# Performance work log

Hardware: AMD Instinct MI355X
Metric: run time of the kernel (lower is better)

Reference implementation:

```python
import jax, jax.numpy as jnp
import numpy as np

DEPTH = 8  # dilation_depth; dilation for layer i is 2**(i % DEPTH)


def causal_conv(x, w, b, dilation):
    # x: [B,C,T], w: [O,I,K] -> causal dilated conv, output [B,O,T]
    pad = (w.shape[-1] - 1) * dilation
    xp = jnp.pad(x, ((0, 0), (0, 0), (pad, 0)))
    y = jax.lax.conv_general_dilated(
        xp, w, window_strides=(1,), padding='VALID',
        rhs_dilation=(dilation,), dimension_numbers=('NCW', 'OIW', 'NCW'))
    return y + b[None, :, None]


def conv1x1(x, w, b):
    # x: [B,C,T], w: [O,C] -> [B,O,T]
    return jnp.einsum('oc,bct->bot', w, x) + b[None, :, None]


def setup_inputs() -> dict:
    key = jax.random.key(0)
    ks = jax.random.split(key, 20)
    B, T, F, E = 16, 2048, 32, 16
    R, S, O, NOUT, L = 256, 128, 64, 24, 32  # residual, skip, out_size, n_output, layers
    s = 0.05
    return {
        'X_batch': jax.random.normal(ks[0], (B, T, F), jnp.float32),
        'X_batch_ex': jax.random.normal(ks[1], (B, E), jnp.float32),
        'w_in': jax.random.normal(ks[2], (R, F, 2), jnp.float32) * s,
        'b_in': jax.random.normal(ks[3], (R,), jnp.float32) * s,
        'w_filter': jax.random.normal(ks[4], (L, R, R, 2), jnp.float32) * s,
        'b_filter': jax.random.normal(ks[5], (L, R), jnp.float32) * s,
        'w_gate': jax.random.normal(ks[6], (L, R, R, 2), jnp.float32) * s,
        'b_gate': jax.random.normal(ks[7], (L, R), jnp.float32) * s,
        'w_res': jax.random.normal(ks[8], (L, R, R), jnp.float32) * s,
        'b_res': jax.random.normal(ks[9], (L, R), jnp.float32) * s,
        'w_skip': jax.random.normal(ks[10], (L, S, R), jnp.float32) * s,
        'b_skip': jax.random.normal(ks[11], (L, S), jnp.float32) * s,
        'w_out1': jax.random.normal(ks[12], (O, S), jnp.float32) * s,
        'b_out1': jax.random.normal(ks[13], (O,), jnp.float32) * s,
        'w_out2': jax.random.normal(ks[14], (O, O), jnp.float32) * s,
        'b_out2': jax.random.normal(ks[15], (O,), jnp.float32) * s,
        'w_lin': jax.random.normal(ks[16], (NOUT, O + E), jnp.float32) * s,
        'b_lin': jax.random.normal(ks[17], (NOUT,), jnp.float32) * s,
    }


def reference(X_batch, X_batch_ex, w_in, b_in, w_filter, b_filter, w_gate, b_gate,
              w_res, b_res, w_skip, b_skip, w_out1, b_out1, w_out2, b_out2,
              w_lin, b_lin):
    # [B,T,F] -> [B,F,T]
    x = jnp.transpose(X_batch, (0, 2, 1))
    x = causal_conv(x, w_in, b_in, 1)
    L = w_filter.shape[0]
    skip_sum = jnp.zeros((x.shape[0], w_skip.shape[1], x.shape[2]), x.dtype)
    for i in range(L):
        d = 2 ** (i % DEPTH)
        f = jnp.tanh(causal_conv(x, w_filter[i], b_filter[i], d))
        g = jax.nn.sigmoid(causal_conv(x, w_gate[i], b_gate[i], d))
        fx = conv1x1(f * g, w_res[i], b_res[i])
        skip_sum = skip_sum + conv1x1(fx, w_skip[i], b_skip[i])
        x = fx + x
    out = jax.nn.relu(skip_sum)
    out = jax.nn.relu(conv1x1(out, w_out1, b_out1))
    out = conv1x1(out, w_out2, b_out2)          # [B,O,T]
    h = out[:, :, -1]                            # last timestep, [B,O]
    h = jnp.concatenate([h, X_batch_ex], axis=1)
    h = jax.nn.relu(h)
    return h @ w_lin.T + b_lin                   # [B, n_output]
```

## Files before the change

kernel.cpp:

```cpp
#include <hip/hip_runtime.h>
#include <cmath>

#define TBUF 1024
#define RCH  256

typedef __bf16 bf16x8 __attribute__((ext_vector_type(8)));
typedef float  f32x4  __attribute__((ext_vector_type(4)));

__device__ inline unsigned short f2bf(float f) {
  unsigned u = __builtin_bit_cast(unsigned, f);
  u += 0x7FFFu + ((u >> 16) & 1u);
  return (unsigned short)(u >> 16);
}
__device__ inline float bf2f(unsigned short h) {
  unsigned u = ((unsigned)h) << 16;
  return __builtin_bit_cast(float, u);
}

__global__ __launch_bounds__(256) void prep(
    const float* __restrict__ wf, const float* __restrict__ wg,
    const float* __restrict__ wr, const float* __restrict__ wsk,
    const float* __restrict__ w_in,
    unsigned short* __restrict__ Wb, unsigned short* __restrict__ Wrb,
    float* __restrict__ wskT, float* __restrict__ w2)
{
  const int bid = blockIdx.x;
  const int tid = threadIdx.x;
  if (bid < 16384) {
    int idx = bid * 256 + tid;
    int c  = idx & 255;
    int op = (idx >> 8) & 511;
    int i  = idx >> 17;
    int o  = op & 255;
    const float* src = (op < 256) ? wf : wg;
    const float2 v = *(const float2*)&src[(((size_t)i * 256 + o) * 256 + c) << 1];
    unsigned short* dst = Wb + ((size_t)i * 512 + op) * 512;
    dst[c]       = f2bf(v.y);
    dst[256 + c] = f2bf(v.x);
  } else if (bid < 18432) {
    int idx = (bid - 16384) * 256 + tid;
    float4 v = ((const float4*)wr)[idx];
    uint2 o;
    o.x = (unsigned)f2bf(v.x) | ((unsigned)f2bf(v.y) << 16);
    o.y = (unsigned)f2bf(v.z) | ((unsigned)f2bf(v.w) << 16);
    ((uint2*)Wrb)[idx] = o;
  } else if (bid < 22528) {
    int idx = (bid - 18432) * 256 + tid;
    int s = idx & 127;
    int c = (idx >> 7) & 255;
    int i = idx >> 15;
    wskT[idx] = wsk[(i * 128 + s) * 256 + c];
  } else {
    int idx = (bid - 22528) * 256 + tid;
    int r = idx & 255;
    int fk = idx >> 8;
    int f = fk & 31, k = fk >> 5;
    w2[idx] = w_in[r * 64 + f * 2 + k];
  }
}

__global__ __launch_bounds__(256) void in_conv(
    const float* __restrict__ X, const float* __restrict__ w2,
    const float* __restrict__ b_in, unsigned short* __restrict__ xbb,
    unsigned short* __restrict__ xlo)
{
  const int bid   = blockIdx.x;
  const int b     = bid & 15;
  const int chunk = bid >> 4;
  const int r     = threadIdx.x;
  __shared__ float Xs[17][32];
  const int tt0 = chunk << 4;
  const int t0  = tt0 + 1024;
  for (int idx = r; idx < 17 * 32; idx += 256) {
    int row = idx >> 5, f = idx & 31;
    Xs[row][f] = X[((size_t)b * 2048 + (t0 - 1 + row)) * 32 + f];
  }
  __syncthreads();
  float w0[32], w1[32];
  #pragma unroll
  for (int f = 0; f < 32; ++f) {
    w0[f] = w2[f * 256 + r];
    w1[f] = w2[(32 + f) * 256 + r];
  }
  const float bias = b_in[r];
  float4 prev[8], cur[8];
  #pragma unroll
  for (int q = 0; q < 8; ++q) prev[q] = *(const float4*)&Xs[0][q * 4];
  #pragma unroll
  for (int j = 0; j < 16; ++j) {
    #pragma unroll
    for (int q = 0; q < 8; ++q) cur[q] = *(const float4*)&Xs[j + 1][q * 4];
    float a = bias;
    #pragma unroll
    for (int q = 0; q < 8; ++q) {
      a = fmaf(w0[q*4+0], prev[q].x, a); a = fmaf(w1[q*4+0], cur[q].x, a);
      a = fmaf(w0[q*4+1], prev[q].y, a); a = fmaf(w1[q*4+1], cur[q].y, a);
      a = fmaf(w0[q*4+2], prev[q].z, a); a = fmaf(w1[q*4+2], cur[q].z, a);
      a = fmaf(w0[q*4+3], prev[q].w, a); a = fmaf(w1[q*4+3], cur[q].w, a);
    }
    int tt = tt0 + j;
    size_t off = ((size_t)b * TBUF + tt) * RCH + r;
    if (tt < 3) { xbb[off] = 0; xlo[off] = 0; }
    else {
      unsigned short hn = f2bf(a);
      xbb[off] = hn;
      xlo[off] = f2bf(a - bf2f(hn));
    }
    #pragma unroll
    for (int q = 0; q < 8; ++q) prev[q] = cur[q];
  }
}

template<int NM>
__global__ __launch_bounds__(1024, 4) void layer_fused(
    const unsigned short* __restrict__ xbb_r, unsigned short* __restrict__ xbb_w,
    unsigned short* __restrict__ xlo,
    const unsigned short* __restrict__ Wb,
    const unsigned short* __restrict__ Wrb,
    const float* __restrict__ bF, const float* __restrict__ bG,
    const float* __restrict__ bR,
    int dd, int t_lo, float* __restrict__ fxs_i)
{
  __shared__ __align__(16) unsigned short As[NM * 16 * 520];
  const int bid  = blockIdx.x;
  const int b    = bid & 15;
  const int tile = bid >> 4;
  const int tid  = threadIdx.x;
  const int w    = tid >> 6;
  const int lane = tid & 63;
  const int l15  = lane & 15;
  const int lk8  = (lane >> 4) << 3;
  const int rr0  = (lane >> 4) << 2;
  const int tt0  = t_lo + tile * (NM * 16);
  const unsigned short* xB = xbb_r + ((size_t)b << 18);

  {
    const int c   = lane;
    const int tap = c >> 5;
    const int cg  = (c & 31) << 3;
    #pragma unroll
    for (int it = 0; it < NM; ++it) {
      int r = it * 16 + w;
      int tt = tt0 + r - tap * dd;
      tt = min(max(tt, 0), 1023);
      __builtin_amdgcn_global_load_lds(
          (const __attribute__((address_space(1))) unsigned int*)
              (xB + ((size_t)tt << 8) + cg),
          (__attribute__((address_space(3))) unsigned int*)
              ((char*)As + r * 1040),
          16, 0, 0);
    }
  }

  const unsigned short* wf0 = Wb + (size_t)(16 * w + l15) * 512 + lk8;
  const unsigned short* wg0 = wf0 + (size_t)256 * 512;
  const unsigned short* wr0 = Wrb + (size_t)(16 * w + l15) * 256 + lk8;
  uint4 nbf = *(const uint4*)(wf0);
  uint4 nbg = *(const uint4*)(wg0);
  uint4 nr0 = *(const uint4*)(wr0);
  __syncthreads();

  f32x4 accf[NM] = {};
  f32x4 accg[NM] = {};
  #pragma unroll 4
  for (int kc = 0; kc < 16; ++kc) {
    uint4 cbf = nbf, cbg = nbg;
    if (kc < 15) {
      nbf = *(const uint4*)(wf0 + (kc + 1) * 32);
      nbg = *(const uint4*)(wg0 + (kc + 1) * 32);
    }
    const int colb = (kc * 32 + lk8) * 2;
    bf16x8 a[NM];
    #pragma unroll
    for (int mf = 0; mf < NM; ++mf)
      a[mf] = *(const bf16x8*)((const char*)As + (mf * 16 + l15) * 1040 + colb);
    bf16x8 vf0 = __builtin_bit_cast(bf16x8, cbf);
    bf16x8 vg0 = __builtin_bit_cast(bf16x8, cbg);
    #pragma unroll
    for (int mf = 0; mf < NM; ++mf) {
      accf[mf] = __builtin_amdgcn_mfma_f32_16x16x32_bf16(a[mf], vf0, accf[mf], 0, 0, 0);
      accg[mf] = __builtin_amdgcn_mfma_f32_16x16x32_bf16(a[mf], vg0, accg[mf], 0, 0, 0);
    }
  }

  const int col = 16 * w + l15;
  float hi_pre[NM][4];
  #pragma unroll
  for (int mf = 0; mf < NM; ++mf)
    #pragma unroll
    for (int j = 0; j < 4; ++j) {
      int row = mf * 16 + rr0 + j;
      hi_pre[mf][j] = bf2f(*(const unsigned short*)((const char*)As + row * 1040 + col * 2));
    }

  unsigned short* xL = xlo + ((size_t)b << 18);
  float lo_pre[NM][4];
  #pragma unroll
  for (int mf = 0; mf < NM; ++mf)
    #pragma unroll
    for (int j = 0; j < 4; ++j) {
      int tt = min(tt0 + mf * 16 + rr0 + j, 1023);
      lo_pre[mf][j] = bf2f(xL[((size_t)tt << 8) + col]);
    }
  __syncthreads();

  unsigned short* Zs = As;
  const float bfv = bF[col];
  const float bgv = bG[col];
  #pragma unroll
  for (int mf = 0; mf < NM; ++mf)
    #pragma unroll
    for (int j = 0; j < 4; ++j) {
      int row = mf * 16 + rr0 + j;
      float pf = accf[mf][j] + bfv;
      float pg = accg[mf][j] + bgv;
      float e2 = __expf(2.f * pf);
      float th = 1.f - 2.f / (e2 + 1.f);
      float sg = 1.f / (1.f + __expf(-pg));
      *(unsigned short*)((char*)Zs + row * 528 + col * 2) = f2bf(th * sg);
    }
  __syncthreads();

  f32x4 acc[NM] = {};
  #pragma unroll 4
  for (int kc = 0; kc < 8; ++kc) {
    uint4 cr0 = nr0;
    if (kc < 7) nr0 = *(const uint4*)(wr0 + (kc + 1) * 32);
    const int colb = (kc * 32 + lk8) * 2;
    bf16x8 a[NM];
    #pragma unroll
    for (int mf = 0; mf < NM; ++mf)
      a[mf] = *(const bf16x8*)((const char*)Zs + (mf * 16 + l15) * 528 + colb);
    bf16x8 v0 = __builtin_bit_cast(bf16x8, cr0);
    #pragma unroll
    for (int mf = 0; mf < NM; ++mf)
      acc[mf] = __builtin_amdgcn_mfma_f32_16x16x32_bf16(a[mf], v0, acc[mf], 0, 0, 0);
  }

  const float brv = bR[col];
  unsigned short* xBb = xbb_w + ((size_t)b << 18);
  #pragma unroll
  for (int mf = 0; mf < NM; ++mf)
    #pragma unroll
    for (int j = 0; j < 4; ++j) {
      int tt = tt0 + mf * 16 + rr0 + j;
      if (tt > 1023) continue;
      size_t off = ((size_t)tt << 8) + col;
      float fx = acc[mf][j] + brv;
      float xn = (hi_pre[mf][j] + lo_pre[mf][j]) + fx;
      unsigned short hn = f2bf(xn);
      xBb[off] = hn;
      xL[off]  = f2bf(xn - bf2f(hn));
      if (tt == 1023) fxs_i[(size_t)b * 256 + col] = fx;
    }
}

__global__ __launch_bounds__(128) void skip_partial(
    const float* __restrict__ fxs, const float* __restrict__ wskT,
    const float* __restrict__ b_skip, float* __restrict__ part)
{
  int i = blockIdx.x, b = blockIdx.y, s = threadIdx.x;
  __shared__ float fxsh[256];
  fxsh[s]       = fxs[((size_t)i * 16 + b) * 256 + s];
  fxsh[s + 128] = fxs[((size_t)i * 16 + b) * 256 + s + 128];
  __syncthreads();
  float a = b_skip[i * 128 + s];
  const float* wp = wskT + (size_t)i * 256 * 128 + s;
  #pragma unroll 4
  for (int c = 0; c < 256; c++)
    a = fmaf(wp[c * 128], fxsh[c], a);
  part[((size_t)i * 16 + b) * 128 + s] = a;
}

__global__ __launch_bounds__(128) void head2(
    const float* __restrict__ part, const float* __restrict__ w_o1,
    const float* __restrict__ b_o1, const float* __restrict__ w_o2,
    const float* __restrict__ b_o2, const float* __restrict__ w_lin,
    const float* __restrict__ b_lin, const float* __restrict__ Xex,
    float* __restrict__ out)
{
  int b = blockIdx.x, tid = threadIdx.x;
  __shared__ float sk[128];
  __shared__ float h1[64];
  __shared__ float hc[80];
  float a = 0.f;
  for (int i = 0; i < 32; i++) a += part[((size_t)i * 16 + b) * 128 + tid];
  sk[tid] = fmaxf(a, 0.f);
  __syncthreads();
  if (tid < 64) {
    float a1 = b_o1[tid];
    for (int s = 0; s < 128; s++) a1 = fmaf(w_o1[tid * 128 + s], sk[s], a1);
    h1[tid] = fmaxf(a1, 0.f);
  }
  __syncthreads();
  if (tid < 64) {
    float a2 = b_o2[tid];
    for (int j = 0; j < 64; j++) a2 = fmaf(w_o2[tid * 64 + j], h1[j], a2);
    hc[tid] = fmaxf(a2, 0.f);
  }
  if (tid >= 64 && tid < 80) hc[tid] = fmaxf(Xex[b * 16 + (tid - 64)], 0.f);
  __syncthreads();
  if (tid < 24) {
    float a3 = b_lin[tid];
    for (int j = 0; j < 80; j++) a3 = fmaf(w_lin[tid * 80 + j], hc[j], a3);
    out[b * 24 + tid] = a3;
  }
}

extern "C" void kernel_launch(void* const* d_in, const int* in_sizes, int n_in,
                              void* d_out, int out_size, void* d_ws, size_t ws_size,
                              hipStream_t stream)
{
  (void)in_sizes; (void)n_in; (void)out_size; (void)ws_size;
  const float* X     = (const float*)d_in[0];
  const float* Xex   = (const float*)d_in[1];
  const float* w_in  = (const float*)d_in[2];
  const float* b_in  = (const float*)d_in[3];
  const float* w_f   = (const float*)d_in[4];
  const float* b_f   = (const float*)d_in[5];
  const float* w_g   = (const float*)d_in[6];
  const float* b_g   = (const float*)d_in[7];
  const float* w_r   = (const float*)d_in[8];
  const float* b_r   = (const float*)d_in[9];
  const float* w_s   = (const float*)d_in[10];
  const float* b_s   = (const float*)d_in[11];
  const float* w_o1  = (const float*)d_in[12];
  const float* b_o1  = (const float*)d_in[13];
  const float* w_o2  = (const float*)d_in[14];
  const float* b_o2  = (const float*)d_in[15];
  const float* w_lin = (const float*)d_in[16];
  const float* b_lin = (const float*)d_in[17];

  float* ws   = (float*)d_ws;
  float* wskT = ws;
  float* fxs  = wskT + 1048576;
  float* part = fxs  + 131072;
  float* w2   = part + 65536;
  unsigned short* Wb   = (unsigned short*)(w2 + 16384);
  unsigned short* Wrb  = Wb   + 8388608;
  unsigned short* xbbA = Wrb  + 2097152;
  unsigned short* xbbB = xbbA + 4194304;
  unsigned short* xlo  = xbbB + 4194304;

  prep<<<22592, 256, 0, stream>>>(w_f, w_g, w_r, w_s, w_in, Wb, Wrb, wskT, w2);
  in_conv<<<1024, 256, 0, stream>>>(X, w2, b_in, xbbA, xlo);

  static const int wI[33] = {1021,1020,1018,1014,1006,990,958,894,
                             766,765,763,759,751,735,703,639,
                             511,510,508,504,496,480,448,384,
                             256,255,253,249,241,225,193,129,1};
  for (int i = 0; i < 32; i++) {
    int dd    = 1 << (i & 7);
    int Wout  = wI[i + 1];
    int t_lo  = TBUF - Wout;
    unsigned short* xin  = (i & 1) ? xbbB : xbbA;
    unsigned short* xout = (i & 1) ? xbbA : xbbB;
    const unsigned short* WbL  = Wb  + (size_t)i * 512 * 512;
    const unsigned short* WrbL = Wrb + (size_t)i * 256 * 256;
    const float* bFi = b_f + i * 256;
    const float* bGi = b_g + i * 256;
    const float* bRi = b_r + i * 256;
    float* fxi = fxs + (size_t)i * 16 * 256;
    int NM = (Wout + 255) >> 8;
    int tiles = (Wout + NM * 16 - 1) / (NM * 16);
    switch (NM) {
      case 4:
        layer_fused<4><<<tiles * 16, 1024, 0, stream>>>(
            xin, xout, xlo, WbL, WrbL, bFi, bGi, bRi, dd, t_lo, fxi);
        break;
      case 3:
        layer_fused<3><<<tiles * 16, 1024, 0, stream>>>(
            xin, xout, xlo, WbL, WrbL, bFi, bGi, bRi, dd, t_lo, fxi);
        break;
      case 2:
        layer_fused<2><<<tiles * 16, 1024, 0, stream>>>(
            xin, xout, xlo, WbL, WrbL, bFi, bGi, bRi, dd, t_lo, fxi);
        break;
      default:
        layer_fused<1><<<tiles * 16, 1024, 0, stream>>>(
            xin, xout, xlo, WbL, WrbL, bFi, bGi, bRi, dd, t_lo, fxi);
        break;
    }
  }
  skip_partial<<<dim3(32, 16), 128, 0, stream>>>(fxs, wskT, b_s, part);
  head2<<<16, 128, 0, stream>>>(part, w_o1, b_o1, w_o2, b_o2, w_lin, b_lin, Xex, (float*)d_out);
}
```

Measured before the change: 883.0 us.

## Fuse pairs of small-dilation WaveNet layers into one kernel with halo recompute

Adds a layer_pair kernel that computes two consecutive residual layers (dilation 1→2 and 4→8) in one launch. It recomputes a 16-row halo of the first layer's output in shared memory, so the intermediate activation never goes through global memory. This cuts launches and global traffic for those layer pairs. In exchange it does redundant halo computation, uses more LDS per block, and double-buffers the lo buffer. The intermediate is kept only in bf16 (the lo part is dropped), which may change precision slightly.

```diff
diff --git a/kernel.cpp b/kernel.cpp
--- a/kernel.cpp
+++ b/kernel.cpp
@@ -15,6 +15,11 @@
 __device__ inline float bf2f(unsigned short h) {
   unsigned u = ((unsigned)h) << 16;
   return __builtin_bit_cast(float, u);
+}
+__device__ __forceinline__ void gl2lds(const unsigned short* g, void* l) {
+  __builtin_amdgcn_global_load_lds(
+      (const __attribute__((address_space(1))) unsigned int*)g,
+      (__attribute__((address_space(3))) unsigned int*)l, 16, 0, 0);
 }
 
 __global__ __launch_bounds__(256) void prep(
@@ -143,15 +148,9 @@
       int r = it * 16 + w;
       int tt = tt0 + r - tap * dd;
       tt = min(max(tt, 0), 1023);
-      __builtin_amdgcn_global_load_lds(
-          (const __attribute__((address_space(1))) unsigned int*)
-              (xB + ((size_t)tt << 8) + cg),
-          (__attribute__((address_space(3))) unsigned int*)
-              ((char*)As + r * 1040),
-          16, 0, 0);
-    }
-  }
-
+      gl2lds(xB + ((size_t)tt << 8) + cg, (char*)As + r * 1040);
+    }
+  }
   const unsigned short* wf0 = Wb + (size_t)(16 * w + l15) * 512 + lk8;
   const unsigned short* wg0 = wf0 + (size_t)256 * 512;
   const unsigned short* wr0 = Wrb + (size_t)(16 * w + l15) * 256 + lk8;
@@ -192,7 +191,6 @@
       int row = mf * 16 + rr0 + j;
       hi_pre[mf][j] = bf2f(*(const unsigned short*)((const char*)As + row * 1040 + col * 2));
     }
-
   unsigned short* xL = xlo + ((size_t)b << 18);
   float lo_pre[NM][4];
   #pragma unroll
@@ -253,6 +251,221 @@
       xL[off]  = f2bf(xn - bf2f(hn));
       if (tt == 1023) fxs_i[(size_t)b * 256 + col] = fx;
     }
+}
+
+template<int D2>
+__global__ __launch_bounds__(1024, 4) void layer_pair(
+    const unsigned short* __restrict__ xhi_r, unsigned short* __restrict__ xhi_w,
+    const unsigned short* __restrict__ xlo_r, unsigned short* __restrict__ xlo_w,
+    const unsigned short* __restrict__ Wb1, const unsigned short* __restrict__ Wrb1,
+    const unsigned short* __restrict__ Wb2, const unsigned short* __restrict__ Wrb2,
+    const float* __restrict__ bF1, const float* __restrict__ bG1,
+    const float* __restrict__ bR1, const float* __restrict__ bF2,
+    const float* __restrict__ bG2, const float* __restrict__ bR2,
+    int dd1, int t_lo2, float* __restrict__ fxs1, float* __restrict__ fxs2)
+{
+  __shared__ __align__(16) unsigned short R1[80 * 520];
+  __shared__ __align__(16) unsigned short R2[80 * 260];
+  const int bid  = blockIdx.x;
+  const int b    = bid & 15;
+  const int tile = bid >> 4;
+  const int tid  = threadIdx.x;
+  const int w    = tid >> 6;
+  const int lane = tid & 63;
+  const int l15  = lane & 15;
+  const int lk8  = (lane >> 4) << 3;
+  const int rr0  = (lane >> 4) << 2;
+  const int tt0e = t_lo2 + tile * 64 - 16;
+  const unsigned short* xH = xhi_r + ((size_t)b << 18);
+  const unsigned short* xL = xlo_r + ((size_t)b << 18);
+
+  {
+    const int c   = lane;
+    const int tap = c >> 5;
+    const int cg  = (c & 31) << 3;
+    #pragma unroll
+    for (int it = 0; it < 5; ++it) {
+      int r = it * 16 + w;
+      int tt = tt0e + r - tap * dd1;
+      tt = min(max(tt, 0), 1023);
+      gl2lds(xH + ((size_t)tt << 8) + cg, (char*)R1 + r * 1040);
+    }
+  }
+  const unsigned short* wf1 = Wb1 + (size_t)(16 * w + l15) * 512 + lk8;
+  const unsigned short* wg1 = wf1 + (size_t)256 * 512;
+  const unsigned short* wr1 = Wrb1 + (size_t)(16 * w + l15) * 256 + lk8;
+  uint4 nbf = *(const uint4*)(wf1);
+  uint4 nbg = *(const uint4*)(wg1);
+  uint4 nr  = *(const uint4*)(wr1);
+  __syncthreads();
+
+  f32x4 accf[5] = {};
+  f32x4 accg[5] = {};
+  #pragma unroll 4
+  for (int kc = 0; kc < 16; ++kc) {
+    uint4 cbf = nbf, cbg = nbg;
+    if (kc < 15) {
+      nbf = *(const uint4*)(wf1 + (kc + 1) * 32);
+      nbg = *(const uint4*)(wg1 + (kc + 1) * 32);
+    }
+    const int colb = (kc * 32 + lk8) * 2;
+    bf16x8 a[5];
+    #pragma unroll
+    for (int mf = 0; mf < 5; ++mf)
+      a[mf] = *(const bf16x8*)((const char*)R1 + (mf * 16 + l15) * 1040 + colb);
+    bf16x8 vf0 = __builtin_bit_cast(bf16x8, cbf);
+    bf16x8 vg0 = __builtin_bit_cast(bf16x8, cbg);
+    #pragma unroll
+    for (int mf = 0; mf < 5; ++mf) {
+      accf[mf] = __builtin_amdgcn_mfma_f32_16x16x32_bf16(a[mf], vf0, accf[mf], 0, 0, 0);
+      accg[mf] = __builtin_amdgcn_mfma_f32_16x16x32_bf16(a[mf], vg0, accg[mf], 0, 0, 0);
+    }
+  }
+
+  const int col = 16 * w + l15;
+  float hi_pre[5][4], lo_pre[5][4];
+  #pragma unroll
+  for (int mf = 0; mf < 5; ++mf)
+    #pragma unroll
+    for (int j = 0; j < 4; ++j) {
+      int row = mf * 16 + rr0 + j;
+      hi_pre[mf][j] = bf2f(*(const unsigned short*)((const char*)R1 + row * 1040 + col * 2));
+      int tt = min(max(tt0e + row, 0), 1023);
+      lo_pre[mf][j] = bf2f(xL[((size_t)tt << 8) + col]);
+    }
+  __syncthreads();
+
+  {
+    const float bfv = bF1[col], bgv = bG1[col];
+    #pragma unroll
+    for (int mf = 0; mf < 5; ++mf)
+      #pragma unroll
+      for (int j = 0; j < 4; ++j) {
+        int row = mf * 16 + rr0 + j;
+        float pf = accf[mf][j] + bfv;
+        float pg = accg[mf][j] + bgv;
+        float e2 = __expf(2.f * pf);
+        float th = 1.f - 2.f / (e2 + 1.f);
+        float sg = 1.f / (1.f + __expf(-pg));
+        *(unsigned short*)((char*)R1 + row * 528 + col * 2) = f2bf(th * sg);
+      }
+  }
+  __syncthreads();
+
+  float xn1[5][4];
+  {
+    f32x4 acc1[5] = {};
+    #pragma unroll 4
+    for (int kc = 0; kc < 8; ++kc) {
+      uint4 cr = nr;
+      if (kc < 7) nr = *(const uint4*)(wr1 + (kc + 1) * 32);
+      const int colb = (kc * 32 + lk8) * 2;
+      bf16x8 a[5];
+      #pragma unroll
+      for (int mf = 0; mf < 5; ++mf)
+        a[mf] = *(const bf16x8*)((const char*)R1 + (mf * 16 + l15) * 528 + colb);
+      bf16x8 v0 = __builtin_bit_cast(bf16x8, cr);
+      #pragma unroll
+      for (int mf = 0; mf < 5; ++mf)
+        acc1[mf] = __builtin_amdgcn_mfma_f32_16x16x32_bf16(a[mf], v0, acc1[mf], 0, 0, 0);
+    }
+    const float br1 = bR1[col];
+    #pragma unroll
+    for (int mf = 0; mf < 5; ++mf)
+      #pragma unroll
+      for (int j = 0; j < 4; ++j) {
+        int row = mf * 16 + rr0 + j;
+        float fx = acc1[mf][j] + br1;
+        float xn = (hi_pre[mf][j] + lo_pre[mf][j]) + fx;
+        xn1[mf][j] = xn;
+        *(unsigned short*)((char*)R2 + row * 520 + col * 2) = f2bf(xn);
+        if (tt0e + row == 1023) fxs1[(size_t)b * 256 + col] = fx;
+      }
+  }
+  const unsigned short* wf2 = Wb2 + (size_t)(16 * w + l15) * 512 + lk8;
+  const unsigned short* wg2 = wf2 + (size_t)256 * 512;
+  const unsigned short* wr2 = Wrb2 + (size_t)(16 * w + l15) * 256 + lk8;
+  nbf = *(const uint4*)(wf2);
+  nbg = *(const uint4*)(wg2);
+  __syncthreads();
+
+  f32x4 acc2f[4] = {};
+  f32x4 acc2g[4] = {};
+  #pragma unroll 4
+  for (int kc = 0; kc < 16; ++kc) {
+    uint4 cbf = nbf, cbg = nbg;
+    if (kc < 15) {
+      nbf = *(const uint4*)(wf2 + (kc + 1) * 32);
+      nbg = *(const uint4*)(wg2 + (kc + 1) * 32);
+    }
+    const int tapofs = (kc >= 8) ? D2 : 0;
+    const int colb = ((kc & 7) * 32 + lk8) * 2;
+    bf16x8 a[4];
+    #pragma unroll
+    for (int mf = 0; mf < 4; ++mf)
+      a[mf] = *(const bf16x8*)((const char*)R2 + (16 + mf * 16 + l15 - tapofs) * 520 + colb);
+    bf16x8 vf0 = __builtin_bit_cast(bf16x8, cbf);
+    bf16x8 vg0 = __builtin_bit_cast(bf16x8, cbg);
+    #pragma unroll
+    for (int mf = 0; mf < 4; ++mf) {
+      acc2f[mf] = __builtin_amdgcn_mfma_f32_16x16x32_bf16(a[mf], vf0, acc2f[mf], 0, 0, 0);
+      acc2g[mf] = __builtin_amdgcn_mfma_f32_16x16x32_bf16(a[mf], vg0, acc2g[mf], 0, 0, 0);
+    }
+  }
+  nr = *(const uint4*)(wr2);
+
+  {
+    const float bfv = bF2[col], bgv = bG2[col];
+    #pragma unroll
+    for (int mf = 0; mf < 4; ++mf)
+      #pragma unroll
+      for (int j = 0; j < 4; ++j) {
+        int row = mf * 16 + rr0 + j;
+        float pf = acc2f[mf][j] + bfv;
+        float pg = acc2g[mf][j] + bgv;
+        float e2 = __expf(2.f * pf);
+        float th = 1.f - 2.f / (e2 + 1.f);
+        float sg = 1.f / (1.f + __expf(-pg));
+        *(unsigned short*)((char*)R1 + row * 528 + col * 2) = f2bf(th * sg);
+      }
+  }
+  __syncthreads();
+
+  {
+    f32x4 acc2[4] = {};
+    #pragma unroll 4
+    for (int kc = 0; kc < 8; ++kc) {
+      uint4 cr = nr;
+      if (kc < 7) nr = *(const uint4*)(wr2 + (kc + 1) * 32);
+      const int colb = (kc * 32 + lk8) * 2;
+      bf16x8 a[4];
+      #pragma unroll
+      for (int mf = 0; mf < 4; ++mf)
+        a[mf] = *(const bf16x8*)((const char*)R1 + (mf * 16 + l15) * 528 + colb);
+      bf16x8 v0 = __builtin_bit_cast(bf16x8, cr);
+      #pragma unroll
+      for (int mf = 0; mf < 4; ++mf)
+        acc2[mf] = __builtin_amdgcn_mfma_f32_16x16x32_bf16(a[mf], v0, acc2[mf], 0, 0, 0);
+    }
+    const float br2 = bR2[col];
+    unsigned short* oH = xhi_w + ((size_t)b << 18);
+    unsigned short* oL = xlo_w + ((size_t)b << 18);
+    #pragma unroll
+    for (int mf = 0; mf < 4; ++mf)
+      #pragma unroll
+      for (int j = 0; j < 4; ++j) {
+        int row = 16 + mf * 16 + rr0 + j;
+        int tt = tt0e + row;
+        if (tt > 1023) continue;
+        size_t off = ((size_t)tt << 8) + col;
+        float fx2 = acc2[mf][j] + br2;
+        float xn2 = xn1[mf + 1][j] + fx2;
+        unsigned short hn = f2bf(xn2);
+        oH[off] = hn;
+        oL[off] = f2bf(xn2 - bf2f(hn));
+        if (tt == 1023) fxs2[(size_t)b * 256 + col] = fx2;
+      }
+  }
 }
 
 __global__ __launch_bounds__(128) void skip_partial(
@@ -338,48 +551,72 @@
   float* w2   = part + 65536;
   unsigned short* Wb   = (unsigned short*)(w2 + 16384);
   unsigned short* Wrb  = Wb   + 8388608;
-  unsigned short* xbbA = Wrb  + 2097152;
-  unsigned short* xbbB = xbbA + 4194304;
-  unsigned short* xlo  = xbbB + 4194304;
+  unsigned short* hiA  = Wrb  + 2097152;
+  unsigned short* hiB  = hiA  + 4194304;
+  unsigned short* loA  = hiB  + 4194304;
+  unsigned short* loB  = loA  + 4194304;
 
   prep<<<22592, 256, 0, stream>>>(w_f, w_g, w_r, w_s, w_in, Wb, Wrb, wskT, w2);
-  in_conv<<<1024, 256, 0, stream>>>(X, w2, b_in, xbbA, xlo);
+  in_conv<<<1024, 256, 0, stream>>>(X, w2, b_in, hiA, loA);
 
   static const int wI[33] = {1021,1020,1018,1014,1006,990,958,894,
                              766,765,763,759,751,735,703,639,
                              511,510,508,504,496,480,448,384,
                              256,255,253,249,241,225,193,129,1};
-  for (int i = 0; i < 32; i++) {
-    int dd    = 1 << (i & 7);
-    int Wout  = wI[i + 1];
-    int t_lo  = TBUF - Wout;
-    unsigned short* xin  = (i & 1) ? xbbB : xbbA;
-    unsigned short* xout = (i & 1) ? xbbA : xbbB;
-    const unsigned short* WbL  = Wb  + (size_t)i * 512 * 512;
-    const unsigned short* WrbL = Wrb + (size_t)i * 256 * 256;
-    const float* bFi = b_f + i * 256;
-    const float* bGi = b_g + i * 256;
-    const float* bRi = b_r + i * 256;
-    float* fxi = fxs + (size_t)i * 16 * 256;
-    int NM = (Wout + 255) >> 8;
-    int tiles = (Wout + NM * 16 - 1) / (NM * 16);
-    switch (NM) {
-      case 4:
-        layer_fused<4><<<tiles * 16, 1024, 0, stream>>>(
-            xin, xout, xlo, WbL, WrbL, bFi, bGi, bRi, dd, t_lo, fxi);
-        break;
-      case 3:
-        layer_fused<3><<<tiles * 16, 1024, 0, stream>>>(
-            xin, xout, xlo, WbL, WrbL, bFi, bGi, bRi, dd, t_lo, fxi);
-        break;
-      case 2:
-        layer_fused<2><<<tiles * 16, 1024, 0, stream>>>(
-            xin, xout, xlo, WbL, WrbL, bFi, bGi, bRi, dd, t_lo, fxi);
-        break;
-      default:
-        layer_fused<1><<<tiles * 16, 1024, 0, stream>>>(
-            xin, xout, xlo, WbL, WrbL, bFi, bGi, bRi, dd, t_lo, fxi);
-        break;
+  unsigned short* hi_c = hiA; unsigned short* hi_n = hiB;
+  unsigned short* lo_c = loA; unsigned short* lo_n = loB;
+  int i = 0;
+  while (i < 32) {
+    const int m = i & 7;
+    if (m == 0 || m == 2) {
+      const int d2   = 1 << ((i + 1) & 7);
+      const int dd1  = 1 << m;
+      const int W2   = wI[i + 2];
+      const int t_lo2 = TBUF - W2;
+      const int tiles = (W2 + 63) / 64;
+      if (d2 == 2)
+        layer_pair<2><<<tiles * 16, 1024, 0, stream>>>(
+            hi_c, hi_n, lo_c, lo_n,
+            Wb + (size_t)i * 262144, Wrb + (size_t)i * 65536,
+            Wb + (size_t)(i + 1) * 262144, Wrb + (size_t)(i + 1) * 65536,
+            b_f + i * 256, b_g + i * 256, b_r + i * 256,
+            b_f + (i + 1) * 256, b_g + (i + 1) * 256, b_r + (i + 1) * 256,
+            dd1, t_lo2, fxs + (size_t)i * 4096, fxs + (size_t)(i + 1) * 4096);
+      else
+        layer_pair<8><<<tiles * 16, 1024, 0, stream>>>(
+            hi_c, hi_n, lo_c, lo_n,
+            Wb + (size_t)i * 262144, Wrb + (size_t)i * 65536,
+            Wb + (size_t)(i + 1) * 262144, Wrb + (size_t)(i + 1) * 65536,
+            b_f + i * 256, b_g + i * 256, b_r + i * 256,
+            b_f + (i + 1) * 256, b_g + (i + 1) * 256, b_r + (i + 1) * 256,
+            dd1, t_lo2, fxs + (size_t)i * 4096, fxs + (size_t)(i + 1) * 4096);
+      { unsigned short* t = hi_c; hi_c = hi_n; hi_n = t; }
+      { unsigned short* t = lo_c; lo_c = lo_n; lo_n = t; }
+      i += 2;
+    } else {
+      const int dd    = 1 << m;
+      const int Wout  = wI[i + 1];
+      const int t_lo  = TBUF - Wout;
+      const int NM    = (Wout + 255) >> 8;
+      const int tiles = (Wout + NM * 16 - 1) / (NM * 16);
+      const unsigned short* WbL  = Wb  + (size_t)i * 262144;
+      const unsigned short* WrbL = Wrb + (size_t)i * 65536;
+      const float* bFi = b_f + i * 256;
+      const float* bGi = b_g + i * 256;
+      const float* bRi = b_r + i * 256;
+      float* fxi = fxs + (size_t)i * 4096;
+      switch (NM) {
+        case 4: layer_fused<4><<<tiles * 16, 1024, 0, stream>>>(
+                    hi_c, hi_n, lo_c, WbL, WrbL, bFi, bGi, bRi, dd, t_lo, fxi); break;
+        case 3: layer_fused<3><<<tiles * 16, 1024, 0, stream>>>(
+                    hi_c, hi_n, lo_c, WbL, WrbL, bFi, bGi, bRi, dd, t_lo, fxi); break;
+        case 2: layer_fused<2><<<tiles * 16, 1024, 0, stream>>>(
+                    hi_c, hi_n, lo_c, WbL, WrbL, bFi, bGi, bRi, dd, t_lo, fxi); break;
+        default: layer_fused<1><<<tiles * 16, 1024, 0, stream>>>(
+                    hi_c, hi_n, lo_c, WbL, WrbL, bFi, bGi, bRi, dd, t_lo, fxi); break;
+      }
+      { unsigned short* t = hi_c; hi_c = hi_n; hi_n = t; }
+      i += 1;
     }
   }
   skip_partial<<<dim3(32, 16), 128, 0, stream>>>(fxs, wskT, b_s, part);
```

After: 941.9 us. 6.7% more time.
